# Kernel tuning notes

Measured on AMD Instinct MI355X. Metric: run time of the kernel, lower is better.

The kernel has to match this reference:

```python
import jax, jax.numpy as jnp
import numpy as np

THRESHOLD = 0.5
NEG_POS = 3
ALPHA = 1.0


def cxcy_to_xy(c):
    return jnp.concatenate([c[..., :2] - c[..., 2:] / 2, c[..., :2] + c[..., 2:] / 2], axis=-1)


def xy_to_cxcy(x):
    return jnp.concatenate([(x[..., :2] + x[..., 2:]) / 2, x[..., 2:] - x[..., :2]], axis=-1)


def encode_gcxgcy(cxcy, priors_cxcy):
    # SSD offset encoding with variances (10, 10, 5, 5)
    return jnp.concatenate([
        (cxcy[..., :2] - priors_cxcy[..., :2]) / (priors_cxcy[..., 2:] / 10.0),
        jnp.log(cxcy[..., 2:] / priors_cxcy[..., 2:]) * 5.0,
    ], axis=-1)


def compute_iou(a, b):
    # a: [n,4] xyxy, b: [m,4] xyxy -> [n,m]
    lt = jnp.maximum(a[:, None, :2], b[None, :, :2])
    rb = jnp.minimum(a[:, None, 2:], b[None, :, 2:])
    wh = jnp.clip(rb - lt, 0.0)
    inter = wh[..., 0] * wh[..., 1]
    area_a = (a[:, 2] - a[:, 0]) * (a[:, 3] - a[:, 1])
    area_b = (b[:, 2] - b[:, 0]) * (b[:, 3] - b[:, 1])
    return inter / (area_a[:, None] + area_b[None, :] - inter)


def _match_one(boxes, labels, db_xy, db_cxcy):
    # boxes: [n_obj,4] xyxy, labels: [n_obj], priors: [P,4]
    n_obj = boxes.shape[0]
    overlaps = compute_iou(boxes, db_xy)                 # [n_obj, P]
    ov_per_box = jnp.max(overlaps, axis=0)               # [P]
    obj_per_box = jnp.argmax(overlaps, axis=0)           # [P]
    box_per_obj = jnp.argmax(overlaps, axis=1)           # [n_obj]
    # force each gt to own its best prior
    obj_per_box = obj_per_box.at[box_per_obj].set(jnp.arange(n_obj))
    ov_per_box = ov_per_box.at[box_per_obj].set(1.0)
    lbl = labels[obj_per_box]                            # [P]
    lbl = jnp.where(ov_per_box < THRESHOLD, 0, lbl)      # background below threshold
    true_locs = encode_gcxgcy(xy_to_cxcy(boxes[obj_per_box]), db_cxcy)  # [P,4]
    return true_locs, lbl


def smooth_l1(x):
    ax = jnp.abs(x)
    return jnp.where(ax < 1.0, 0.5 * x * x, ax - 0.5)


def reference(loc_pred, cls_pred, gt_boxes, gt_labels, default_boxes):
    # loc_pred: [B,P,4], cls_pred: [B,P,C], gt_boxes: [B,n_obj,4],
    # gt_labels: [B,n_obj] int, default_boxes: [P,4] cxcywh
    db_xy = cxcy_to_xy(default_boxes)
    true_locs, true_labels = jax.vmap(_match_one, in_axes=(0, 0, None, None))(
        gt_boxes, gt_labels, db_xy, default_boxes)      # [B,P,4], [B,P]

    positive = true_labels > 0                           # [B,P]
    n_pos = jnp.sum(positive, axis=1)                    # [B]
    n_pos_total = jnp.sum(n_pos).astype(loc_pred.dtype)

    # localization loss: SmoothL1 mean over positive box elements
    loc_elem = smooth_l1(loc_pred - true_locs)           # [B,P,4]
    loc_loss = jnp.sum(loc_elem * positive[..., None]) / (n_pos_total * 4.0)

    # confidence loss: cross entropy with 3:1 hard negative mining
    logp = jax.nn.log_softmax(cls_pred, axis=-1)         # [B,P,C]
    ce = -jnp.take_along_axis(logp, true_labels[..., None], axis=-1)[..., 0]  # [B,P]
    conf_pos = jnp.sum(ce * positive)
    ce_neg = jnp.where(positive, 0.0, ce)
    # rank negatives by loss (descending) per image; take top neg_pos * n_pos
    ranks = jnp.argsort(jnp.argsort(-ce_neg, axis=1), axis=1)  # [B,P]
    hard_neg = ranks < (NEG_POS * n_pos)[:, None]
    conf_hard = jnp.sum(ce_neg * hard_neg)
    conf_loss = (conf_pos + conf_hard) / n_pos_total

    return conf_loss + ALPHA * loc_loss


def setup_inputs() -> dict:
    key = jax.random.key(0)
    ks = jax.random.split(key, 8)
    B, P, C, n_obj = 64, 8732, 81, 32

    # priors in cxcywh, valid in [0,1]
    db_cxy = jax.random.uniform(ks[0], (P, 2), minval=0.05, maxval=0.95)
    db_wh = jax.random.uniform(ks[1], (P, 2), minval=0.05, maxval=0.3)
    default_boxes = jnp.concatenate([db_cxy, db_wh], axis=-1).astype(jnp.float32)

    # gt boxes: valid xyxy built from centers and sizes
    g_cxy = jax.random.uniform(ks[2], (B, n_obj, 2), minval=0.2, maxval=0.8)
    g_wh = jax.random.uniform(ks[3], (B, n_obj, 2), minval=0.1, maxval=0.4)
    gt_boxes = jnp.concatenate([g_cxy - g_wh / 2, g_cxy + g_wh / 2], axis=-1).astype(jnp.float32)
    gt_labels = jax.random.randint(ks[4], (B, n_obj), 1, C)

    loc_pred = jax.random.normal(ks[5], (B, P, 4), dtype=jnp.float32) * 0.1
    cls_pred = jax.random.normal(ks[6], (B, P, C), dtype=jnp.float32)

    return {"loc_pred": loc_pred, "cls_pred": cls_pred, "gt_boxes": gt_boxes,
            "gt_labels": gt_labels, "default_boxes": default_boxes}
```

## Files before the change

kernel.cpp:

```cpp
#include <hip/hip_runtime.h>
#include <hip/hip_bf16.h>
#include <math.h>

#define BB 64
#define PP 8732
#define CC 81
#define NOBJ 32
#define CHUNKS ((PP + 255) / 256)
#define NPRI (BB * PP)
#define WTILE 16
#define WTW (WTILE * CC)
#define NWT (NPRI / WTILE)
#define LSE_BLOCKS 1792
#define BP_BLOCKS (BB * NOBJ)
#define PRE_BLOCKS (BP_BLOCKS + LSE_BLOCKS)

typedef float f4 __attribute__((ext_vector_type(4)));

__device__ __forceinline__ float sl1(float x) {
    float ax = fabsf(x);
    return (ax < 1.0f) ? 0.5f * x * x : ax - 0.5f;
}

__global__ __launch_bounds__(256) void k_pre(
    const float* __restrict__ gt_boxes,
    const float* __restrict__ dbox,
    const float* __restrict__ cls_pred,
    int*   __restrict__ bp,
    float* __restrict__ lsex0,
    float* __restrict__ acc,
    int*   __restrict__ npt,
    int*   __restrict__ done,
    int*   __restrict__ n_pos)
{
    __shared__ float s_x[4][WTW];
    __shared__ float s_bv[4];
    __shared__ int   s_bi[4];
    const int tid  = threadIdx.x;
    const int wave = tid >> 6, lane = tid & 63;

    if (blockIdx.x == 0) {
        if (tid < BB) n_pos[tid] = 0;
        else if (tid < BB + 3) acc[tid - BB] = 0.0f;
        else if (tid == BB + 3) *npt = 0;
        else if (tid == BB + 4) *done = 0;
    }

    if (blockIdx.x < BP_BLOCKS) {
        const int b = blockIdx.x >> 5;
        const int o = blockIdx.x & 31;

        const float* g = gt_boxes + (b * NOBJ + o) * 4;
        float gx0 = g[0], gy0 = g[1], gx1 = g[2], gy1 = g[3];
        float garea = (gx1 - gx0) * (gy1 - gy0);

        float best = -1.0f; int bpp = 0x7fffffff;
        for (int p = tid; p < PP; p += 256) {
            float4 db = reinterpret_cast<const float4*>(dbox)[p];
            float px0 = db.x - db.z * 0.5f, py0 = db.y - db.w * 0.5f;
            float px1 = db.x + db.z * 0.5f, py1 = db.y + db.w * 0.5f;
            float parea = db.z * db.w;
            float lx = fmaxf(px0, gx0), ly = fmaxf(py0, gy0);
            float rx = fminf(px1, gx1), ry = fminf(py1, gy1);
            float w = fmaxf(rx - lx, 0.0f), h = fmaxf(ry - ly, 0.0f);
            float inter = w * h;
            float iou = inter / (garea + parea - inter);
            if (iou > best) { best = iou; bpp = p; }
        }
#pragma unroll
        for (int m = 32; m > 0; m >>= 1) {
            float ov = __shfl_xor(best, m);
            int   op = __shfl_xor(bpp, m);
            if (ov > best || (ov == best && op < bpp)) { best = ov; bpp = op; }
        }
        if (lane == 0) { s_bv[wave] = best; s_bi[wave] = bpp; }
        __syncthreads();
        if (tid == 0) {
            for (int w2 = 1; w2 < 4; ++w2) {
                if (s_bv[w2] > best || (s_bv[w2] == best && s_bi[w2] < bpp)) {
                    best = s_bv[w2]; bpp = s_bi[w2];
                }
            }
            bp[b * NOBJ + o] = bpp;
        }
        return;
    }

    const int rloc = lane >> 2, q = lane & 3;
    const int NW   = LSE_BLOCKS * 4;
    float* sx = s_x[wave];
    f4* dst = reinterpret_cast<f4*>(sx);

    const float L2E = 1.4426950408889634f;
    const float LN2 = 0.6931471805599453f;

    int wt = (blockIdx.x - BP_BLOCKS) * 4 + wave;
    f4 r0, r1, r2, r3, r4, r5;
    if (wt < NWT) {
        const f4* src = reinterpret_cast<const f4*>(cls_pred + (size_t)wt * WTW);
        r0 = __builtin_nontemporal_load(src + lane);
        r1 = __builtin_nontemporal_load(src + 64 + lane);
        r2 = __builtin_nontemporal_load(src + 128 + lane);
        r3 = __builtin_nontemporal_load(src + 192 + lane);
        r4 = __builtin_nontemporal_load(src + 256 + lane);
        if (lane < 4) r5 = __builtin_nontemporal_load(src + 320 + lane);
    }

    while (wt < NWT) {
        dst[lane] = r0; dst[64 + lane] = r1; dst[128 + lane] = r2;
        dst[192 + lane] = r3; dst[256 + lane] = r4;
        if (lane < 4) dst[320 + lane] = r5;
        const int pidx = wt * WTILE + rloc;

        wt += NW;
        if (wt < NWT) {
            const f4* src = reinterpret_cast<const f4*>(cls_pred + (size_t)wt * WTW);
            r0 = __builtin_nontemporal_load(src + lane);
            r1 = __builtin_nontemporal_load(src + 64 + lane);
            r2 = __builtin_nontemporal_load(src + 128 + lane);
            r3 = __builtin_nontemporal_load(src + 192 + lane);
            r4 = __builtin_nontemporal_load(src + 256 + lane);
            if (lane < 4) r5 = __builtin_nontemporal_load(src + 320 + lane);
        }

        const float* x = sx + rloc * CC;
        const int base = q * 20;
        float s0 = 0.0f, s1 = 0.0f;
#pragma unroll
        for (int j = 0; j < 20; j += 2) {
            s0 += exp2f(x[base + j]     * L2E);
            s1 += exp2f(x[base + j + 1] * L2E);
        }
        float s = s0 + s1;
        if (q == 3) s += exp2f(x[80] * L2E);
        s += __shfl_xor(s, 1);
        s += __shfl_xor(s, 2);

        if (q == 0) {
            float2 o;
            o.x = log2f(s) * LN2;
            o.y = x[0];
            reinterpret_cast<float2*>(lsex0)[pidx] = o;
        }
    }
}

__global__ __launch_bounds__(256) void k_assign(
    const float* __restrict__ loc_pred,
    const float* __restrict__ gt_boxes,
    const int*   __restrict__ gt_labels,
    const float* __restrict__ dbox,
    const int*   __restrict__ bp,
    const float* __restrict__ cls_pred,
    const float* __restrict__ lsex0,
    float* __restrict__ ce_neg,
    int*   __restrict__ n_pos,
    float* __restrict__ acc,
    int*   __restrict__ n_pos_total)
{
    __shared__ float s_gx0[NOBJ], s_gy0[NOBJ], s_gx1[NOBJ], s_gy1[NOBJ], s_garea[NOBJ];
    __shared__ float s_gcx[NOBJ], s_gcy[NOBJ], s_gw[NOBJ], s_gh[NOBJ];
    __shared__ int   s_glbl[NOBJ], s_bp[NOBJ];
    __shared__ float red_f[256], red_g[256];
    __shared__ int   red_i[256];

    const int b     = blockIdx.x / CHUNKS;
    const int chunk = blockIdx.x % CHUNKS;
    const int tid   = threadIdx.x;
    const int p     = chunk * 256 + tid;

    if (tid < NOBJ) {
        float x0 = gt_boxes[(b * NOBJ + tid) * 4 + 0];
        float y0 = gt_boxes[(b * NOBJ + tid) * 4 + 1];
        float x1 = gt_boxes[(b * NOBJ + tid) * 4 + 2];
        float y1 = gt_boxes[(b * NOBJ + tid) * 4 + 3];
        s_gx0[tid] = x0; s_gy0[tid] = y0; s_gx1[tid] = x1; s_gy1[tid] = y1;
        s_garea[tid] = (x1 - x0) * (y1 - y0);
        s_gcx[tid] = (x0 + x1) * 0.5f;
        s_gcy[tid] = (y0 + y1) * 0.5f;
        s_gw[tid]  = x1 - x0;
        s_gh[tid]  = y1 - y0;
        s_glbl[tid] = gt_labels[b * NOBJ + tid];
        s_bp[tid]   = bp[b * NOBJ + tid];
    }
    __syncthreads();

    float loc_local = 0.0f, pos_local = 0.0f;
    int   np_local  = 0;

    if (p < PP) {
        const int idx = b * PP + p;
        float4 db = reinterpret_cast<const float4*>(dbox)[p];
        float px0 = db.x - db.z * 0.5f, py0 = db.y - db.w * 0.5f;
        float px1 = db.x + db.z * 0.5f, py1 = db.y + db.w * 0.5f;
        float parea = db.z * db.w;

        float best = -1.0f; int bo = 0;
#pragma unroll
        for (int o = 0; o < NOBJ; ++o) {
            float lx = fmaxf(px0, s_gx0[o]), ly = fmaxf(py0, s_gy0[o]);
            float rx = fminf(px1, s_gx1[o]), ry = fminf(py1, s_gy1[o]);
            float w = fmaxf(rx - lx, 0.0f), h = fmaxf(ry - ly, 0.0f);
            float inter = w * h;
            float iou = inter / (s_garea[o] + parea - inter);
            if (iou > best) { best = iou; bo = o; }
        }
        int forced = -1;
#pragma unroll
        for (int o = 0; o < NOBJ; ++o)
            if (s_bp[o] == p) forced = o;

        int o_use, lbl;
        if (forced >= 0) { o_use = forced; lbl = s_glbl[forced]; }
        else             { o_use = bo; lbl = (best < 0.5f) ? 0 : s_glbl[bo]; }

        float2 lx0 = reinterpret_cast<const float2*>(lsex0)[idx];

        if (lbl > 0) {
            np_local = 1;
            ce_neg[idx] = 0.0f;
            float xl = cls_pred[(size_t)idx * CC + lbl];
            pos_local = fmaxf(lx0.x - xl, 0.0f);
            float g0 = (s_gcx[o_use] - db.x) / (db.z / 10.0f);
            float g1 = (s_gcy[o_use] - db.y) / (db.w / 10.0f);
            float g2 = logf(s_gw[o_use] / db.z) * 5.0f;
            float g3 = logf(s_gh[o_use] / db.w) * 5.0f;
            float4 lp = reinterpret_cast<const float4*>(loc_pred)[idx];
            loc_local = sl1(lp.x - g0) + sl1(lp.y - g1) + sl1(lp.z - g2) + sl1(lp.w - g3);
        } else {
            ce_neg[idx] = fmaxf(lx0.x - lx0.y, 0.0f);
        }
    }

    red_f[tid] = loc_local;
    red_g[tid] = pos_local;
    red_i[tid] = np_local;
    __syncthreads();
#pragma unroll
    for (int st = 128; st > 0; st >>= 1) {
        if (tid < st) {
            red_f[tid] += red_f[tid + st];
            red_g[tid] += red_g[tid + st];
            red_i[tid] += red_i[tid + st];
        }
        __syncthreads();
    }
    if (tid == 0) {
        if (red_f[0] != 0.0f) atomicAdd(&acc[0], red_f[0]);
        if (red_g[0] != 0.0f) atomicAdd(&acc[1], red_g[0]);
        if (red_i[0]) {
            atomicAdd(&n_pos[b], red_i[0]);
            atomicAdd(n_pos_total, red_i[0]);
        }
    }
}

__global__ __launch_bounds__(1024) void k_select(
    const float* __restrict__ ce_neg,
    const int*   __restrict__ n_pos,
    float* __restrict__ acc,
    const int*  __restrict__ n_pos_total,
    int*   __restrict__ done,
    float* __restrict__ out)
{
    __shared__ unsigned int sv[PP];
    __shared__ unsigned int h16[16][256];
    __shared__ unsigned int hist[257];
    __shared__ unsigned int wtot[4];
    __shared__ unsigned int s_prefix, s_krem;
    __shared__ float rf[16];
    __shared__ int   ri[16];

    const int b = blockIdx.x, tid = threadIdx.x;
    const int lane = tid & 63, w = tid >> 6;

    int K = n_pos[b] * 3;
    if (K > PP) K = PP;

    if (K > 0) {
        for (int i = tid; i < PP; i += 1024)
            sv[i] = __float_as_uint(ce_neg[b * PP + i]);

        unsigned int prefix = 0, krem = (unsigned int)K;
        for (int shift = 24; shift >= 0; shift -= 8) {
            unsigned int* hflat = &h16[0][0];
            for (int j = tid; j < 16 * 256; j += 1024) hflat[j] = 0;
            if (tid == 0) hist[256] = 0;
            __syncthreads();
            unsigned int mask_hi = (shift == 24) ? 0u : (0xFFFFFFFFu << (shift + 8));
            for (int i = tid; i < PP; i += 1024) {
                unsigned int v = sv[i];
                if ((v & mask_hi) == prefix)
                    atomicAdd(&h16[w][(v >> shift) & 0xFFu], 1u);
            }
            __syncthreads();
            unsigned int s = 0;
            if (tid < 256) {
#pragma unroll
                for (int r = 0; r < 16; ++r) s += h16[r][tid];
#pragma unroll
                for (int off = 1; off < 64; off <<= 1) {
                    unsigned int a = __shfl_down(s, off);
                    if (lane + off < 64) s += a;
                }
                if (lane == 0) wtot[w] = s;
            }
            __syncthreads();
            if (tid < 256) {
                unsigned int sb = 0;
#pragma unroll
                for (int r = 0; r < 16; ++r) sb += h16[r][tid];
                unsigned int suf = sb;
#pragma unroll
                for (int off = 1; off < 64; off <<= 1) {
                    unsigned int a = __shfl_down(suf, off);
                    if (lane + off < 64) suf += a;
                }
                for (int w2 = w + 1; w2 < 4; ++w2) suf += wtot[w2];
                hist[tid] = suf;
            }
            __syncthreads();
            if (tid < 256) {
                unsigned int suf  = hist[tid];
                unsigned int suf1 = hist[tid + 1];
                if (suf >= krem && suf1 < krem) {
                    s_prefix = prefix | ((unsigned int)tid << shift);
                    s_krem   = krem - suf1;
                }
            }
            __syncthreads();
            prefix = s_prefix; krem = s_krem;
        }
        float cutoff = __uint_as_float(prefix);

        float sum_gt = 0.0f; int cnt_gt = 0;
        for (int i = tid; i < PP; i += 1024) {
            float v = __uint_as_float(sv[i]);
            if (v > cutoff) { sum_gt += v; cnt_gt++; }
        }
#pragma unroll
        for (int m = 32; m > 0; m >>= 1) {
            sum_gt += __shfl_xor(sum_gt, m);
            cnt_gt += __shfl_xor(cnt_gt, m);
        }
        if (lane == 0) { rf[w] = sum_gt; ri[w] = cnt_gt; }
        __syncthreads();
        if (tid == 0) {
            float sg = 0.0f; int cg = 0;
#pragma unroll
            for (int r = 0; r < 16; ++r) { sg += rf[r]; cg += ri[r]; }
            atomicAdd(&acc[2], sg + (float)(K - cg) * cutoff);
        }
    }

    if (tid == 0) {
        __threadfence();
        int old = atomicAdd(done, 1);
        if (old == BB - 1) {
            float a0 = atomicAdd(&acc[0], 0.0f);
            float a1 = atomicAdd(&acc[1], 0.0f);
            float a2 = atomicAdd(&acc[2], 0.0f);
            float npt = (float)atomicAdd((int*)n_pos_total, 0);
            out[0] = (a1 + a2) / npt + a0 / (npt * 4.0f);
        }
    }
}

extern "C" void kernel_launch(void* const* d_in, const int* in_sizes, int n_in,
                              void* d_out, int out_size, void* d_ws, size_t ws_size,
                              hipStream_t stream) {
    const float* loc_pred  = (const float*)d_in[0];
    const float* cls_pred  = (const float*)d_in[1];
    const float* gt_boxes  = (const float*)d_in[2];
    const int*   gt_labels = (const int*)d_in[3];
    const float* dbox      = (const float*)d_in[4];
    float* out = (float*)d_out;

    float* acc    = (float*)d_ws;
    int*   npt    = (int*)d_ws + 3;
    int*   done   = (int*)d_ws + 4;
    int*   n_pos  = (int*)d_ws + 8;
    int*   bp     = (int*)d_ws + 8 + BB;
    float* lsex0  = (float*)((int*)d_ws + 8 + BB + BB * NOBJ);
    float* ce_neg = lsex0 + (size_t)2 * NPRI;

    k_pre<<<PRE_BLOCKS, 256, 0, stream>>>(gt_boxes, dbox, cls_pred,
                                          bp, lsex0, acc, npt, done, n_pos);
    k_assign<<<BB * CHUNKS, 256, 0, stream>>>(loc_pred, gt_boxes, gt_labels, dbox, bp,
                                              cls_pred, lsex0, ce_neg, n_pos, acc, npt);
    k_select<<<BB, 1024, 0, stream>>>(ce_neg, n_pos, acc, npt, done, out);
}
```

Baseline: 160.8 us.

## Split log-sum-exp into separate kernel reading rows directly without shared staging

The fused pre-kernel is split into a standalone log-sum-exp kernel and a separate best-prior kernel. The LSE kernel now has each quad of lanes load its own unaligned 81-float row segment straight into registers with masked edge elements, replacing the cooperative nontemporal load, shared-memory staging and software prefetch. It also writes the background CE directly, so the assign kernel no longer reads x0 or writes ce_neg for negatives. The cost is an extra kernel launch, lost overlap between the IoU search and the LSE pass, and less coalesced, partly redundant 16-byte loads.

```diff
diff --git a/kernel.cpp b/kernel.cpp
--- a/kernel.cpp
+++ b/kernel.cpp
@@ -11,9 +11,7 @@
 #define WTILE 16
 #define WTW (WTILE * CC)
 #define NWT (NPRI / WTILE)
-#define LSE_BLOCKS 1792
-#define BP_BLOCKS (BB * NOBJ)
-#define PRE_BLOCKS (BP_BLOCKS + LSE_BLOCKS)
+#define CE_BLOCKS 2048
 
 typedef float f4 __attribute__((ext_vector_type(4)));
 
@@ -22,22 +20,81 @@
     return (ax < 1.0f) ? 0.5f * x * x : ax - 0.5f;
 }
 
-__global__ __launch_bounds__(256) void k_pre(
+__global__ __launch_bounds__(256) void k_ce(
+    const float* __restrict__ cls_pred,
+    float* __restrict__ lse,
+    float* __restrict__ ce_neg)
+{
+    const int tid  = threadIdx.x;
+    const int wave = tid >> 6, lane = tid & 63;
+    const int rloc = lane >> 2, q = lane & 3;
+    const int NW   = CE_BLOCKS * 4;
+
+    const int seg_start = rloc * CC + q * 20;
+    const int seg_len   = (q == 3) ? 21 : 20;
+    const int ws        = seg_start >> 2;
+    const int a         = seg_start & 3;
+    const int hi_cnt    = a + seg_len - 20;
+
+    const float L2E = 1.4426950408889634f;
+    const float LN2 = 0.6931471805599453f;
+
+    for (int wt = blockIdx.x * 4 + wave; wt < NWT; wt += NW) {
+        const f4* src = reinterpret_cast<const f4*>(cls_pred) + (size_t)wt * (WTW / 4) + ws;
+        f4 w0 = src[0];
+        f4 w1 = src[1];
+        f4 w2 = src[2];
+        f4 w3 = src[3];
+        f4 w4 = src[4];
+        f4 w5 = src[5];
+
+        float s0 = 0.0f, s1 = 0.0f;
+#pragma unroll
+        for (int k = 0; k < 4; ++k) {
+            float e = exp2f(w0[k] * L2E);
+            s0 += (k >= a) ? e : 0.0f;
+        }
+#pragma unroll
+        for (int k = 0; k < 4; ++k) s1 += exp2f(w1[k] * L2E);
+#pragma unroll
+        for (int k = 0; k < 4; ++k) s0 += exp2f(w2[k] * L2E);
+#pragma unroll
+        for (int k = 0; k < 4; ++k) s1 += exp2f(w3[k] * L2E);
+#pragma unroll
+        for (int k = 0; k < 4; ++k) s0 += exp2f(w4[k] * L2E);
+#pragma unroll
+        for (int k = 0; k < 4; ++k) {
+            float e = exp2f(w5[k] * L2E);
+            s1 += (k < hi_cnt) ? e : 0.0f;
+        }
+        float s = s0 + s1;
+        s += __shfl_xor(s, 1);
+        s += __shfl_xor(s, 2);
+
+        if (q == 0) {
+            float x0 = w0[a];
+            float l  = log2f(s) * LN2;
+            const int pidx = wt * WTILE + rloc;
+            lse[pidx]    = l;
+            ce_neg[pidx] = fmaxf(l - x0, 0.0f);
+        }
+    }
+}
+
+__global__ __launch_bounds__(256) void k_bestprior(
     const float* __restrict__ gt_boxes,
     const float* __restrict__ dbox,
-    const float* __restrict__ cls_pred,
     int*   __restrict__ bp,
-    float* __restrict__ lsex0,
     float* __restrict__ acc,
     int*   __restrict__ npt,
     int*   __restrict__ done,
     int*   __restrict__ n_pos)
 {
-    __shared__ float s_x[4][WTW];
     __shared__ float s_bv[4];
     __shared__ int   s_bi[4];
-    const int tid  = threadIdx.x;
-    const int wave = tid >> 6, lane = tid & 63;
+    const int tid = threadIdx.x, lane = tid & 63, wave = tid >> 6;
+    const int b = blockIdx.x >> 5;
+    const int o = blockIdx.x & 31;
 
     if (blockIdx.x == 0) {
         if (tid < BB) n_pos[tid] = 0;
@@ -46,102 +103,38 @@
         else if (tid == BB + 4) *done = 0;
     }
 
-    if (blockIdx.x < BP_BLOCKS) {
-        const int b = blockIdx.x >> 5;
-        const int o = blockIdx.x & 31;
-
-        const float* g = gt_boxes + (b * NOBJ + o) * 4;
-        float gx0 = g[0], gy0 = g[1], gx1 = g[2], gy1 = g[3];
-        float garea = (gx1 - gx0) * (gy1 - gy0);
-
-        float best = -1.0f; int bpp = 0x7fffffff;
-        for (int p = tid; p < PP; p += 256) {
-            float4 db = reinterpret_cast<const float4*>(dbox)[p];
-            float px0 = db.x - db.z * 0.5f, py0 = db.y - db.w * 0.5f;
-            float px1 = db.x + db.z * 0.5f, py1 = db.y + db.w * 0.5f;
-            float parea = db.z * db.w;
-            float lx = fmaxf(px0, gx0), ly = fmaxf(py0, gy0);
-            float rx = fminf(px1, gx1), ry = fminf(py1, gy1);
-            float w = fmaxf(rx - lx, 0.0f), h = fmaxf(ry - ly, 0.0f);
-            float inter = w * h;
-            float iou = inter / (garea + parea - inter);
-            if (iou > best) { best = iou; bpp = p; }
-        }
-#pragma unroll
-        for (int m = 32; m > 0; m >>= 1) {
-            float ov = __shfl_xor(best, m);
-            int   op = __shfl_xor(bpp, m);
-            if (ov > best || (ov == best && op < bpp)) { best = ov; bpp = op; }
-        }
-        if (lane == 0) { s_bv[wave] = best; s_bi[wave] = bpp; }
-        __syncthreads();
-        if (tid == 0) {
-            for (int w2 = 1; w2 < 4; ++w2) {
-                if (s_bv[w2] > best || (s_bv[w2] == best && s_bi[w2] < bpp)) {
-                    best = s_bv[w2]; bpp = s_bi[w2];
-                }
-            }
-            bp[b * NOBJ + o] = bpp;
-        }
-        return;
-    }
-
-    const int rloc = lane >> 2, q = lane & 3;
-    const int NW   = LSE_BLOCKS * 4;
-    float* sx = s_x[wave];
-    f4* dst = reinterpret_cast<f4*>(sx);
-
-    const float L2E = 1.4426950408889634f;
-    const float LN2 = 0.6931471805599453f;
-
-    int wt = (blockIdx.x - BP_BLOCKS) * 4 + wave;
-    f4 r0, r1, r2, r3, r4, r5;
-    if (wt < NWT) {
-        const f4* src = reinterpret_cast<const f4*>(cls_pred + (size_t)wt * WTW);
-        r0 = __builtin_nontemporal_load(src + lane);
-        r1 = __builtin_nontemporal_load(src + 64 + lane);
-        r2 = __builtin_nontemporal_load(src + 128 + lane);
-        r3 = __builtin_nontemporal_load(src + 192 + lane);
-        r4 = __builtin_nontemporal_load(src + 256 + lane);
-        if (lane < 4) r5 = __builtin_nontemporal_load(src + 320 + lane);
-    }
-
-    while (wt < NWT) {
-        dst[lane] = r0; dst[64 + lane] = r1; dst[128 + lane] = r2;
-        dst[192 + lane] = r3; dst[256 + lane] = r4;
-        if (lane < 4) dst[320 + lane] = r5;
-        const int pidx = wt * WTILE + rloc;
-
-        wt += NW;
-        if (wt < NWT) {
-            const f4* src = reinterpret_cast<const f4*>(cls_pred + (size_t)wt * WTW);
-            r0 = __builtin_nontemporal_load(src + lane);
-            r1 = __builtin_nontemporal_load(src + 64 + lane);
-            r2 = __builtin_nontemporal_load(src + 128 + lane);
-            r3 = __builtin_nontemporal_load(src + 192 + lane);
-            r4 = __builtin_nontemporal_load(src + 256 + lane);
-            if (lane < 4) r5 = __builtin_nontemporal_load(src + 320 + lane);
-        }
-
-        const float* x = sx + rloc * CC;
-        const int base = q * 20;
-        float s0 = 0.0f, s1 = 0.0f;
-#pragma unroll
-        for (int j = 0; j < 20; j += 2) {
-            s0 += exp2f(x[base + j]     * L2E);
-            s1 += exp2f(x[base + j + 1] * L2E);
-        }
-        float s = s0 + s1;
-        if (q == 3) s += exp2f(x[80] * L2E);
-        s += __shfl_xor(s, 1);
-        s += __shfl_xor(s, 2);
-
-        if (q == 0) {
-            float2 o;
-            o.x = log2f(s) * LN2;
-            o.y = x[0];
-            reinterpret_cast<float2*>(lsex0)[pidx] = o;
-        }
+    const float* g = gt_boxes + (b * NOBJ + o) * 4;
+    float gx0 = g[0], gy0 = g[1], gx1 = g[2], gy1 = g[3];
+    float garea = (gx1 - gx0) * (gy1 - gy0);
+
+    float best = -1.0f; int bpp = 0x7fffffff;
+    for (int p = tid; p < PP; p += 256) {
+        float4 db = reinterpret_cast<const float4*>(dbox)[p];
+        float px0 = db.x - db.z * 0.5f, py0 = db.y - db.w * 0.5f;
+        float px1 = db.x + db.z * 0.5f, py1 = db.y + db.w * 0.5f;
+        float parea = db.z * db.w;
+        float lx = fmaxf(px0, gx0), ly = fmaxf(py0, gy0);
+        float rx = fminf(px1, gx1), ry = fminf(py1, gy1);
+        float w = fmaxf(rx - lx, 0.0f), h = fmaxf(ry - ly, 0.0f);
+        float inter = w * h;
+        float iou = inter / (garea + parea - inter);
+        if (iou > best) { best = iou; bpp = p; }
+    }
+#pragma unroll
+    for (int m = 32; m > 0; m >>= 1) {
+        float ov = __shfl_xor(best, m);
+        int   op = __shfl_xor(bpp, m);
+        if (ov > best || (ov == best && op < bpp)) { best = ov; bpp = op; }
+    }
+    if (lane == 0) { s_bv[wave] = best; s_bi[wave] = bpp; }
+    __syncthreads();
+    if (tid == 0) {
+        for (int w2 = 1; w2 < 4; ++w2) {
+            if (s_bv[w2] > best || (s_bv[w2] == best && s_bi[w2] < bpp)) {
+                best = s_bv[w2]; bpp = s_bi[w2];
+            }
+        }
+        bp[b * NOBJ + o] = bpp;
     }
 }
 
@@ -152,7 +145,7 @@
     const float* __restrict__ dbox,
     const int*   __restrict__ bp,
     const float* __restrict__ cls_pred,
-    const float* __restrict__ lsex0,
+    const float* __restrict__ lse,
     float* __restrict__ ce_neg,
     int*   __restrict__ n_pos,
     float* __restrict__ acc,
@@ -214,21 +207,17 @@
         if (forced >= 0) { o_use = forced; lbl = s_glbl[forced]; }
         else             { o_use = bo; lbl = (best < 0.5f) ? 0 : s_glbl[bo]; }
 
-        float2 lx0 = reinterpret_cast<const float2*>(lsex0)[idx];
-
         if (lbl > 0) {
             np_local = 1;
             ce_neg[idx] = 0.0f;
             float xl = cls_pred[(size_t)idx * CC + lbl];
-            pos_local = fmaxf(lx0.x - xl, 0.0f);
+            pos_local = fmaxf(lse[idx] - xl, 0.0f);
             float g0 = (s_gcx[o_use] - db.x) / (db.z / 10.0f);
             float g1 = (s_gcy[o_use] - db.y) / (db.w / 10.0f);
             float g2 = logf(s_gw[o_use] / db.z) * 5.0f;
             float g3 = logf(s_gh[o_use] / db.w) * 5.0f;
             float4 lp = reinterpret_cast<const float4*>(loc_pred)[idx];
             loc_local = sl1(lp.x - g0) + sl1(lp.y - g1) + sl1(lp.z - g2) + sl1(lp.w - g3);
-        } else {
-            ce_neg[idx] = fmaxf(lx0.x - lx0.y, 0.0f);
         }
     }
 
@@ -381,12 +370,13 @@
     int*   done   = (int*)d_ws + 4;
     int*   n_pos  = (int*)d_ws + 8;
     int*   bp     = (int*)d_ws + 8 + BB;
-    float* lsex0  = (float*)((int*)d_ws + 8 + BB + BB * NOBJ);
-    float* ce_neg = lsex0 + (size_t)2 * NPRI;
-
-    k_pre<<<PRE_BLOCKS, 256, 0, stream>>>(gt_boxes, dbox, cls_pred,
-                                          bp, lsex0, acc, npt, done, n_pos);
+    float* lse    = (float*)((int*)d_ws + 8 + BB + BB * NOBJ);
+    float* ce_neg = lse + (size_t)NPRI;
+
+    k_ce<<<CE_BLOCKS, 256, 0, stream>>>(cls_pred, lse, ce_neg);
+    k_bestprior<<<BB * NOBJ, 256, 0, stream>>>(gt_boxes, dbox, bp,
+                                               acc, npt, done, n_pos);
     k_assign<<<BB * CHUNKS, 256, 0, stream>>>(loc_pred, gt_boxes, gt_labels, dbox, bp,
-                                              cls_pred, lsex0, ce_neg, n_pos, acc, npt);
+                                              cls_pred, lse, ce_neg, n_pos, acc, npt);
     k_select<<<BB, 1024, 0, stream>>>(ce_neg, n_pos, acc, npt, done, out);
 }
```

After: 164.9 us. +2.5%, slower.
